# Optimization experiments

Measured on AMD Instinct MI355X. Metric: run time of the kernel, lower is better.

The kernel has to match this reference:

```python
import jax, jax.numpy as jnp
from jax import lax
import numpy as np

B = 262144   # batch of independent series
K = 64       # forecast horizon (init k)
D_IN = 200   # Non_AR_net input dim (Linear(200,100))
H = 100      # hidden width


def setup_inputs() -> dict:
    key = jax.random.key(0)
    ks = jax.random.split(key, 10)
    f32 = jnp.float32
    x = jax.random.normal(ks[0], (B, D_IN), f32)
    last_mu = jax.random.normal(ks[1], (B,), f32)
    # last_sigma is the variance state; keep it strictly positive
    last_sigma = jax.random.uniform(ks[2], (B,), f32) + 0.5
    # MLP params (Kaiming-ish scale)
    W1 = jax.random.normal(ks[3], (D_IN, H), f32) / np.float32(np.sqrt(D_IN))
    b1 = jnp.zeros((H,), f32)
    W2 = jax.random.normal(ks[4], (H, H), f32) / np.float32(np.sqrt(H))
    b2 = jnp.zeros((H,), f32)
    W3 = jax.random.normal(ks[5], (H, K), f32) / np.float32(np.sqrt(H))
    b3 = jnp.zeros((K,), f32)
    return {
        "x": x, "last_mu": last_mu, "last_sigma": last_sigma,
        "alpha_mu": jnp.asarray(0.1, f32), "alpha_sigma": jnp.asarray(0.1, f32),
        "beta_mu": jnp.asarray(0.9, f32), "beta_sigma": jnp.asarray(0.85, f32),
        "omega_mu": jnp.asarray(0.0, f32), "omega_sigma": jnp.asarray(0.05, f32),
        "nu": jnp.asarray(5.0, f32), "norm_strength": jnp.asarray(1.0, f32),
        "W1": W1, "b1": b1, "W2": W2, "b2": b2, "W3": W3, "b3": b3,
    }


def _mlp(x, W1, b1, W2, b2, W3, b3):
    h = jax.nn.relu(x @ W1 + b1)
    h = jax.nn.relu(h @ W2 + b2)
    return h @ W3 + b3  # [B, K]


def _ar_gas(deep_preds, last_mu, last_sigma, a_mu, a_s, b_mu, b_s, o_mu, o_s, nu, ns):
    """Student-t score-driven (GAS) k-step recurrence, vectorized over batch.
    deep_preds: [B, K]; state mu, sigma2: [B]."""
    w = 1.0 + 1.0 / nu

    def step(carry, y):  # y: [B]
        mu, s2 = carry
        e = y - mu
        denom = 1.0 + e * e / (nu * s2)
        mu_new = o_mu + ns * a_mu * (w * e / denom) + b_mu * mu
        s2_new = o_s + ns * a_s * (w * e * e / denom - s2) + b_s * s2
        return (mu_new, s2_new), (mu_new, s2_new)

    (_, _), (mus, s2s) = lax.scan(step, (last_mu, last_sigma), deep_preds.T)
    return mus.T, jnp.sqrt(s2s.T)  # [B, K] each


def reference(x, last_mu, last_sigma, alpha_mu, alpha_sigma, beta_mu, beta_sigma,
              omega_mu, omega_sigma, nu, norm_strength,
              W1, b1, W2, b2, W3, b3):
    deep_preds = _mlp(x, W1, b1, W2, b2, W3, b3)            # [B, K]
    dp = lax.stop_gradient(deep_preds)                       # .detach() in torch
    mu_pred, sigma_pred = _ar_gas(dp, last_mu, last_sigma,
                                  alpha_mu, alpha_sigma, beta_mu, beta_sigma,
                                  omega_mu, omega_sigma, nu, norm_strength)
    return deep_preds * sigma_pred + mu_pred                 # [B, K]
```

## Files before the change

### kernel.cpp

```cpp
#include <hip/hip_runtime.h>
#include <hip/hip_bf16.h>

typedef short v8s __attribute__((ext_vector_type(8)));
typedef float v4f __attribute__((ext_vector_type(4)));

#define THREADS 512
#define WAVES   8
#define NTILES  4
#define BMROWS  512
#define W1F     0
#define W2F     49
#define W3F     77
#define SLABB   95232
#define SLAB_STRIDE 264
#define SLAB_SIZE   4224
#define LDS_TOTAL   (SLABB + WAVES * SLAB_SIZE)

__device__ __forceinline__ unsigned short f2bf(float f) {
    union { __hip_bfloat16 h; unsigned short u; } c;
    c.h = __float2bfloat16(f);
    return c.u;
}
__device__ __forceinline__ unsigned pk2(float a, float b) {
    return (unsigned)f2bf(a) | ((unsigned)f2bf(b) << 16);
}
__device__ __forceinline__ v4f mfma16(v8s a, v8s b, v4f c) {
    return __builtin_amdgcn_mfma_f32_16x16x32_bf16(a, b, c, 0, 0, 0);
}
__device__ __forceinline__ v8s mkfrag(float4 a, float4 b) {
    union { unsigned u[4]; v8s s; } t;
    t.u[0] = pk2(a.x, a.y); t.u[1] = pk2(a.z, a.w);
    t.u[2] = pk2(b.x, b.y); t.u[3] = pk2(b.z, b.w);
    return t.s;
}
__device__ __forceinline__ void gload_lds16(const void* g, void* l) {
    __builtin_amdgcn_global_load_lds(
        (const __attribute__((address_space(1))) void*)g,
        (__attribute__((address_space(3))) void*)l, 16, 0, 0);
}

__global__ void prep_weights(const float* __restrict__ W1,
                             const float* __restrict__ W2,
                             const float* __restrict__ W3,
                             uint4* __restrict__ wf) {
    const int bid = blockIdx.x, l = threadIdx.x;
    const float* W; int K, N, KC, base, f;
    if (bid < 49)      { W = W1; K = 200; N = 100; KC = 7; base = W1F * 64; f = bid; }
    else if (bid < 77) { W = W2; K = 100; N = 100; KC = 4; base = W2F * 64; f = bid - 49; }
    else               { W = W3; K = 100; N = 64;  KC = 4; base = W3F * 64; f = bid - 77; }
    const int kc = f % KC;
    const int n  = (f / KC) * 16 + (l & 15);
    unsigned u[4];
    #pragma unroll
    for (int p = 0; p < 4; ++p) {
        const int k0 = kc * 32 + (l >> 4) * 8 + p * 2;
        const float a = (k0     < K && n < N) ? W[(size_t)k0 * N + n]       : 0.f;
        const float b = (k0 + 1 < K && n < N) ? W[(size_t)(k0 + 1) * N + n] : 0.f;
        u[p] = pk2(a, b);
    }
    wf[base + f * 64 + l] = make_uint4(u[0], u[1], u[2], u[3]);
}

__global__ __launch_bounds__(THREADS, 2)
void ar_gas_v18(const float* __restrict__ x,
                const float* __restrict__ last_mu,
                const float* __restrict__ last_sigma,
                const float* __restrict__ p_amu, const float* __restrict__ p_as,
                const float* __restrict__ p_bmu, const float* __restrict__ p_bs,
                const float* __restrict__ p_omu, const float* __restrict__ p_os,
                const float* __restrict__ p_nu,  const float* __restrict__ p_ns,
                const float* __restrict__ b1, const float* __restrict__ b2,
                const float* __restrict__ b3,
                const uint4* __restrict__ wf,
                float* __restrict__ out)
{
    extern __shared__ __align__(16) unsigned char L[];
    const int tid  = threadIdx.x;
    const int lane = tid & 63;
    const int wid  = tid >> 6;
    const int l15  = lane & 15;
    const int l4   = lane >> 4;
    const int blk  = blockIdx.x;

    const float anu = *p_nu,  ans = *p_ns;
    const float aMu = *p_amu, aSg = *p_as;
    const float bMu = *p_bmu, bSg = *p_bs;
    const float oMu = *p_omu, oSg = *p_os;
    const float wS  = 1.f + __builtin_amdgcn_rcpf(anu);
    const float cmu = ans * aMu * wS;
    const float cs  = ans * aSg * wS;
    const float bs2 = bSg - ans * aSg;

#define XLOADT(dst, base_row, kk)                                       \
    { int kb = (kk) * 32 + l4 * 8;                                      \
      kb = (kb + 8 <= 200) ? kb : 168;     \
      const float* p_ = x + ((base_row) + l15) * 200;                   \
      dst[kk][0] = *(const float4*)(p_ + kb);                           \
      dst[kk][1] = *(const float4*)(p_ + kb + 4); }

    const size_t gw0 = (size_t)blk * BMROWS + (size_t)wid * 64;

    float4 xv[7][2];
    #pragma unroll
    for (int kc = 0; kc < 7; ++kc) XLOADT(xv, gw0, kc);

    for (int s = wid; s < 93; s += WAVES)
        gload_lds16(wf + s * 64 + lane, L + s * 1024);
    __syncthreads();

#define FRAG_W1(f)  (*(const uint4*)(&L[(W1F + (f)) * 1024 + lane * 16]))
#define FRAG_W2(f)  (*(const uint4*)(&L[(W2F + (f)) * 1024 + lane * 16]))
#define FRAG_W3(f)  (*(const uint4*)(&L[(W3F + (f)) * 1024 + lane * 16]))

    const int sb      = SLABB + wid * SLAB_SIZE;
    const int sb_epi  = sb + (l4 * 4) * SLAB_STRIDE + l15 * 2;
    const int sb_rd   = sb + l15 * SLAB_STRIDE + l4 * 16;
    const int sb_dpw  = sb + (l4 * 4) * SLAB_STRIDE + l15 * 4;
    const int sb_gas  = sb + l15 * SLAB_STRIDE;
    const int sb_st   = sb + l4 * SLAB_STRIDE + l15 * 16;

    #pragma unroll 1
    for (int t = 0; t < NTILES; ++t) {
        const size_t gw = gw0 + t * 16;

        const float mu_init = last_mu[gw + l15];
        const float s2_init = last_sigma[gw + l15];

        v4f acc[7];
        #pragma unroll
        for (int nt = 0; nt < 7; ++nt) acc[nt] = (v4f){0.f, 0.f, 0.f, 0.f};
        #pragma unroll
        for (int kc = 0; kc < 7; ++kc) {
            uint4 bu[7];
            #pragma unroll
            for (int nt = 0; nt < 7; ++nt) bu[nt] = FRAG_W1(nt * 7 + kc);
            const v8s af = mkfrag(xv[kc][0], xv[kc][1]);
            #pragma unroll
            for (int nt = 0; nt < 7; ++nt)
                acc[nt] = mfma16(af, *(const v8s*)&bu[nt], acc[nt]);
        }

        if (t < NTILES - 1) {
            #pragma unroll
            for (int kc = 0; kc < 7; ++kc) XLOADT(xv, gw0 + (t + 1) * 16, kc);
        }

        {
            float bv[7];
            #pragma unroll
            for (int nt = 0; nt < 7; ++nt) {
                const int c = nt * 16 + l15;
                bv[nt] = (c < 100) ? b1[c] : 0.f;
            }
            #pragma unroll
            for (int nt = 0; nt < 7; ++nt)
                #pragma unroll
                for (int r = 0; r < 4; ++r) {
                    const float v = fmaxf(acc[nt][r] + bv[nt], 0.f);
                    *(unsigned short*)(&L[sb_epi + r * SLAB_STRIDE + nt * 32]) =
                        f2bf(v);
                }
        }
        if (lane < 32)
            *(uint4*)(&L[sb + (lane >> 1) * SLAB_STRIDE + 224 + (lane & 1) * 16]) =
                make_uint4(0, 0, 0, 0);

        v4f acc2[7];
        #pragma unroll
        for (int nt = 0; nt < 7; ++nt) acc2[nt] = (v4f){0.f, 0.f, 0.f, 0.f};
        #pragma unroll
        for (int kc = 0; kc < 4; ++kc) {
            uint4 bu[7];
            #pragma unroll
            for (int nt = 0; nt < 7; ++nt) bu[nt] = FRAG_W2(nt * 4 + kc);
            uint4 t0 = *(const uint4*)(&L[sb_rd + kc * 64]);
            const v8s af = *(v8s*)&t0;
            #pragma unroll
            for (int nt = 0; nt < 7; ++nt)
                acc2[nt] = mfma16(af, *(const v8s*)&bu[nt], acc2[nt]);
        }
        {
            float bv[7];
            #pragma unroll
            for (int nt = 0; nt < 7; ++nt) {
                const int c = nt * 16 + l15;
                bv[nt] = (c < 100) ? b2[c] : 0.f;
            }
            #pragma unroll
            for (int nt = 0; nt < 7; ++nt)
                #pragma unroll
                for (int r = 0; r < 4; ++r) {
                    const float v = fmaxf(acc2[nt][r] + bv[nt], 0.f);
                    *(unsigned short*)(&L[sb_epi + r * SLAB_STRIDE + nt * 32]) =
                        f2bf(v);
                }
        }

        v4f acc3[4];
        #pragma unroll
        for (int nt = 0; nt < 4; ++nt) acc3[nt] = (v4f){0.f, 0.f, 0.f, 0.f};
        #pragma unroll
        for (int kc = 0; kc < 4; ++kc) {
            uint4 bu[4];
            #pragma unroll
            for (int nt = 0; nt < 4; ++nt) bu[nt] = FRAG_W3(nt * 4 + kc);
            uint4 t0 = *(const uint4*)(&L[sb_rd + kc * 64]);
            const v8s af = *(v8s*)&t0;
            #pragma unroll
            for (int nt = 0; nt < 4; ++nt)
                acc3[nt] = mfma16(af, *(const v8s*)&bu[nt], acc3[nt]);
        }
        {
            float bv[4];
            #pragma unroll
            for (int nt = 0; nt < 4; ++nt) bv[nt] = b3[nt * 16 + l15];
            #pragma unroll
            for (int nt = 0; nt < 4; ++nt)
                #pragma unroll
                for (int r = 0; r < 4; ++r)
                    *(float*)(&L[sb_dpw + r * SLAB_STRIDE + nt * 64]) =
                        acc3[nt][r] + bv[nt];
        }

        if (lane < 16) {
            float mu = mu_init;
            float s2 = s2_init;
#define GAS_STEP(Y, O)                                                  \
            {   const float e    = (Y) - mu;                            \
                const float nus2 = anu * s2;                            \
                const float den  = fmaf(e, e, nus2);                    \
                const float r0   = __builtin_amdgcn_rcpf(den);          \
                const float p    = e * nus2 * r0;                       \
                mu = fmaf(cmu, p, fmaf(bMu, mu, oMu));                  \
                s2 = fmaf(cs, e * p, fmaf(bs2, s2, oSg));               \
                (O) = fmaf((Y), __builtin_amdgcn_sqrtf(s2), mu); }
            #pragma unroll
            for (int q = 0; q < 16; ++q) {
                float4 d = *(float4*)(&L[sb_gas + q * 16]);
                float o0, o1, o2, o3;
                GAS_STEP(d.x, o0); GAS_STEP(d.y, o1);
                GAS_STEP(d.z, o2); GAS_STEP(d.w, o3);
                *(float4*)(&L[sb_gas + q * 16]) = make_float4(o0, o1, o2, o3);
            }
#undef GAS_STEP
        }

        #pragma unroll
        for (int i = 0; i < 4; ++i) {
            float4 v = *(float4*)(&L[sb_st + i * (4 * SLAB_STRIDE)]);
            ((float4*)out)[gw * 16 + i * 64 + lane] = v;
        }
    }
#undef FRAG_W1
#undef FRAG_W2
#undef FRAG_W3
#undef XLOADT
}

extern "C" void kernel_launch(void* const* d_in, const int* in_sizes, int n_in,
                              void* d_out, int out_size, void* d_ws, size_t ws_size,
                              hipStream_t stream) {
    const float* x          = (const float*)d_in[0];
    const float* last_mu    = (const float*)d_in[1];
    const float* last_sigma = (const float*)d_in[2];
    const float* amu        = (const float*)d_in[3];
    const float* asig       = (const float*)d_in[4];
    const float* bmu        = (const float*)d_in[5];
    const float* bsig       = (const float*)d_in[6];
    const float* omu        = (const float*)d_in[7];
    const float* osig       = (const float*)d_in[8];
    const float* nu         = (const float*)d_in[9];
    const float* ns         = (const float*)d_in[10];
    const float* W1         = (const float*)d_in[11];
    const float* b1         = (const float*)d_in[12];
    const float* W2         = (const float*)d_in[13];
    const float* b2         = (const float*)d_in[14];
    const float* W3         = (const float*)d_in[15];
    const float* b3         = (const float*)d_in[16];
    float* out = (float*)d_out;

    uint4* wf = (uint4*)d_ws;
    prep_weights<<<93, 64, 0, stream>>>(W1, W2, W3, wf);

    hipFuncSetAttribute((const void*)ar_gas_v18,
                        hipFuncAttributeMaxDynamicSharedMemorySize, LDS_TOTAL);

    const int B = in_sizes[1];
    dim3 grid(B / BMROWS), block(THREADS);
    ar_gas_v18<<<grid, block, LDS_TOTAL, stream>>>(
        x, last_mu, last_sigma,
        amu, asig, bmu, bsig, omu, osig, nu, ns,
        b1, b2, b3, wf, out);
}
```

Before: 83.29 us.

## Split fused MLP+GAS kernel into MLP kernel and per-row scan kernel

```diff
diff --git a/kernel.cpp b/kernel.cpp
--- a/kernel.cpp
+++ b/kernel.cpp
@@ -4,17 +4,17 @@
 typedef short v8s __attribute__((ext_vector_type(8)));
 typedef float v4f __attribute__((ext_vector_type(4)));
 
-#define THREADS 512
-#define WAVES   8
-#define NTILES  4
-#define BMROWS  512
+#define A_THREADS 1024
+#define A_WAVES   16
+#define A_NTILES  4
+#define A_ROWS    1024
 #define W1F     0
 #define W2F     49
 #define W3F     77
 #define SLABB   95232
-#define SLAB_STRIDE 264
-#define SLAB_SIZE   4224
-#define LDS_TOTAL   (SLABB + WAVES * SLAB_SIZE)
+#define SLAB_STRIDE 260
+#define SLAB_SIZE   4160
+#define LDS_TOTAL   (SLABB + A_WAVES * SLAB_SIZE)
 
 __device__ __forceinline__ unsigned short f2bf(float f) {
     union { __hip_bfloat16 h; unsigned short u; } c;
@@ -61,18 +61,12 @@
     wf[base + f * 64 + l] = make_uint4(u[0], u[1], u[2], u[3]);
 }
 
-__global__ __launch_bounds__(THREADS, 2)
-void ar_gas_v18(const float* __restrict__ x,
-                const float* __restrict__ last_mu,
-                const float* __restrict__ last_sigma,
-                const float* __restrict__ p_amu, const float* __restrict__ p_as,
-                const float* __restrict__ p_bmu, const float* __restrict__ p_bs,
-                const float* __restrict__ p_omu, const float* __restrict__ p_os,
-                const float* __restrict__ p_nu,  const float* __restrict__ p_ns,
-                const float* __restrict__ b1, const float* __restrict__ b2,
-                const float* __restrict__ b3,
-                const uint4* __restrict__ wf,
-                float* __restrict__ out)
+__global__ __launch_bounds__(A_THREADS, 4)
+void ar_mlp(const float* __restrict__ x,
+            const float* __restrict__ b1, const float* __restrict__ b2,
+            const float* __restrict__ b3,
+            const uint4* __restrict__ wf,
+            float* __restrict__ dp)
 {
     extern __shared__ __align__(16) unsigned char L[];
     const int tid  = threadIdx.x;
@@ -82,29 +76,21 @@
     const int l4   = lane >> 4;
     const int blk  = blockIdx.x;
 
-    const float anu = *p_nu,  ans = *p_ns;
-    const float aMu = *p_amu, aSg = *p_as;
-    const float bMu = *p_bmu, bSg = *p_bs;
-    const float oMu = *p_omu, oSg = *p_os;
-    const float wS  = 1.f + __builtin_amdgcn_rcpf(anu);
-    const float cmu = ans * aMu * wS;
-    const float cs  = ans * aSg * wS;
-    const float bs2 = bSg - ans * aSg;
-
-#define XLOADT(dst, base_row, kk)                                       \
+#define XLOAD(d0, d1, base_row, kk)                                     \
     { int kb = (kk) * 32 + l4 * 8;                                      \
       kb = (kb + 8 <= 200) ? kb : 168;     \
       const float* p_ = x + ((base_row) + l15) * 200;                   \
-      dst[kk][0] = *(const float4*)(p_ + kb);                           \
-      dst[kk][1] = *(const float4*)(p_ + kb + 4); }
-
-    const size_t gw0 = (size_t)blk * BMROWS + (size_t)wid * 64;
-
-    float4 xv[7][2];
-    #pragma unroll
-    for (int kc = 0; kc < 7; ++kc) XLOADT(xv, gw0, kc);
-
-    for (int s = wid; s < 93; s += WAVES)
+      d0 = *(const float4*)(p_ + kb);                                   \
+      d1 = *(const float4*)(p_ + kb + 4); }
+
+    const size_t gw0 = (size_t)blk * A_ROWS + (size_t)wid * 64;
+
+    float4 xv[3][2];
+    XLOAD(xv[0][0], xv[0][1], gw0, 0);
+    XLOAD(xv[1][0], xv[1][1], gw0, 1);
+    XLOAD(xv[2][0], xv[2][1], gw0, 2);
+
+    for (int s = wid; s < 93; s += A_WAVES)
         gload_lds16(wf + s * 64 + lane, L + s * 1024);
     __syncthreads();
 
@@ -115,16 +101,10 @@
     const int sb      = SLABB + wid * SLAB_SIZE;
     const int sb_epi  = sb + (l4 * 4) * SLAB_STRIDE + l15 * 2;
     const int sb_rd   = sb + l15 * SLAB_STRIDE + l4 * 16;
-    const int sb_dpw  = sb + (l4 * 4) * SLAB_STRIDE + l15 * 4;
-    const int sb_gas  = sb + l15 * SLAB_STRIDE;
-    const int sb_st   = sb + l4 * SLAB_STRIDE + l15 * 16;
 
     #pragma unroll 1
-    for (int t = 0; t < NTILES; ++t) {
+    for (int t = 0; t < A_NTILES; ++t) {
         const size_t gw = gw0 + t * 16;
-
-        const float mu_init = last_mu[gw + l15];
-        const float s2_init = last_sigma[gw + l15];
 
         v4f acc[7];
         #pragma unroll
@@ -134,15 +114,16 @@
             uint4 bu[7];
             #pragma unroll
             for (int nt = 0; nt < 7; ++nt) bu[nt] = FRAG_W1(nt * 7 + kc);
-            const v8s af = mkfrag(xv[kc][0], xv[kc][1]);
+            const v8s af = mkfrag(xv[kc % 3][0], xv[kc % 3][1]);
+            if (kc < 4) XLOAD(xv[kc % 3][0], xv[kc % 3][1], gw, kc + 3);
             #pragma unroll
             for (int nt = 0; nt < 7; ++nt)
                 acc[nt] = mfma16(af, *(const v8s*)&bu[nt], acc[nt]);
         }
-
-        if (t < NTILES - 1) {
-            #pragma unroll
-            for (int kc = 0; kc < 7; ++kc) XLOADT(xv, gw0 + (t + 1) * 16, kc);
+        if (t < A_NTILES - 1) {
+            XLOAD(xv[0][0], xv[0][1], gw + 16, 0);
+            XLOAD(xv[1][0], xv[1][1], gw + 16, 1);
+            XLOAD(xv[2][0], xv[2][1], gw + 16, 2);
         }
 
         {
@@ -218,43 +199,66 @@
             for (int nt = 0; nt < 4; ++nt)
                 #pragma unroll
                 for (int r = 0; r < 4; ++r)
-                    *(float*)(&L[sb_dpw + r * SLAB_STRIDE + nt * 64]) =
+                    dp[(gw + l4 * 4 + r) * 64 + nt * 16 + l15] =
                         acc3[nt][r] + bv[nt];
-        }
-
-        if (lane < 16) {
-            float mu = mu_init;
-            float s2 = s2_init;
-#define GAS_STEP(Y, O)                                                  \
-            {   const float e    = (Y) - mu;                            \
-                const float nus2 = anu * s2;                            \
-                const float den  = fmaf(e, e, nus2);                    \
-                const float r0   = __builtin_amdgcn_rcpf(den);          \
-                const float p    = e * nus2 * r0;                       \
-                mu = fmaf(cmu, p, fmaf(bMu, mu, oMu));                  \
-                s2 = fmaf(cs, e * p, fmaf(bs2, s2, oSg));               \
-                (O) = fmaf((Y), __builtin_amdgcn_sqrtf(s2), mu); }
-            #pragma unroll
-            for (int q = 0; q < 16; ++q) {
-                float4 d = *(float4*)(&L[sb_gas + q * 16]);
-                float o0, o1, o2, o3;
-                GAS_STEP(d.x, o0); GAS_STEP(d.y, o1);
-                GAS_STEP(d.z, o2); GAS_STEP(d.w, o3);
-                *(float4*)(&L[sb_gas + q * 16]) = make_float4(o0, o1, o2, o3);
-            }
-#undef GAS_STEP
-        }
-
-        #pragma unroll
-        for (int i = 0; i < 4; ++i) {
-            float4 v = *(float4*)(&L[sb_st + i * (4 * SLAB_STRIDE)]);
-            ((float4*)out)[gw * 16 + i * 64 + lane] = v;
         }
     }
 #undef FRAG_W1
 #undef FRAG_W2
 #undef FRAG_W3
-#undef XLOADT
+#undef XLOAD
+}
+
+__global__ void ar_gas_scan(float* __restrict__ io,
+                            const float* __restrict__ last_mu,
+                            const float* __restrict__ last_sigma,
+                            const float* __restrict__ p_amu,
+                            const float* __restrict__ p_as,
+                            const float* __restrict__ p_bmu,
+                            const float* __restrict__ p_bs,
+                            const float* __restrict__ p_omu,
+                            const float* __restrict__ p_os,
+                            const float* __restrict__ p_nu,
+                            const float* __restrict__ p_ns)
+{
+    const int row = blockIdx.x * 256 + threadIdx.x;
+    float4* rp = (float4*)(io + (size_t)row * 64);
+
+    const float anu = *p_nu,  ans = *p_ns;
+    const float aMu = *p_amu, aSg = *p_as;
+    const float bMu = *p_bmu, bSg = *p_bs;
+    const float oMu = *p_omu, oSg = *p_os;
+    const float w   = 1.f + __builtin_amdgcn_rcpf(anu);
+    const float cmu = ans * aMu * w;
+    const float cs  = ans * aSg * w;
+    const float bs2 = bSg - ans * aSg;
+
+    float mu = last_mu[row];
+    float s2 = last_sigma[row];
+
+    float4 c[16];
+    c[0] = rp[0]; c[1] = rp[1];
+
+#define GAS_STEP(Y, O)                                                  \
+    {   const float e    = (Y) - mu;                                    \
+        const float nus2 = anu * s2;                                    \
+        const float den  = fmaf(e, e, nus2);                            \
+        const float r0   = __builtin_amdgcn_rcpf(den);                  \
+        const float p    = e * nus2 * r0;                               \
+        mu = fmaf(cmu, p, fmaf(bMu, mu, oMu));                          \
+        s2 = fmaf(cs, e * p, fmaf(bs2, s2, oSg));                       \
+        (O) = fmaf((Y), __builtin_amdgcn_sqrtf(s2), mu); }
+
+    #pragma unroll
+    for (int q = 0; q < 16; ++q) {
+        if (q + 2 < 16) c[q + 2] = rp[q + 2];
+        float4 d = c[q];
+        float o0, o1, o2, o3;
+        GAS_STEP(d.x, o0); GAS_STEP(d.y, o1);
+        GAS_STEP(d.z, o2); GAS_STEP(d.w, o3);
+        rp[q] = make_float4(o0, o1, o2, o3);
+    }
+#undef GAS_STEP
 }
 
 extern "C" void kernel_launch(void* const* d_in, const int* in_sizes, int n_in,
@@ -282,13 +286,13 @@
     uint4* wf = (uint4*)d_ws;
     prep_weights<<<93, 64, 0, stream>>>(W1, W2, W3, wf);
 
-    hipFuncSetAttribute((const void*)ar_gas_v18,
+    hipFuncSetAttribute((const void*)ar_mlp,
                         hipFuncAttributeMaxDynamicSharedMemorySize, LDS_TOTAL);
 
     const int B = in_sizes[1];
-    dim3 grid(B / BMROWS), block(THREADS);
-    ar_gas_v18<<<grid, block, LDS_TOTAL, stream>>>(
-        x, last_mu, last_sigma,
-        amu, asig, bmu, bsig, omu, osig, nu, ns,
-        b1, b2, b3, wf, out);
-}
+    ar_mlp<<<dim3(B / A_ROWS), dim3(A_THREADS), LDS_TOTAL, stream>>>(
+        x, b1, b2, b3, wf, out);
+    ar_gas_scan<<<dim3(B / 256), dim3(256), 0, stream>>>(
+        out, last_mu, last_sigma,
+        amu, asig, bmu, bsig, omu, osig, nu, ns);
+}
```

Measured after the change: 131.9 us. 58.3% more time.

## Software-pipeline GAS recurrence of previous tile into next tile's layer-1 MFMA loop

Applied to the files above, without the earlier changes.

```diff
diff --git a/kernel.cpp b/kernel.cpp
--- a/kernel.cpp
+++ b/kernel.cpp
@@ -62,7 +62,7 @@
 }
 
 __global__ __launch_bounds__(THREADS, 2)
-void ar_gas_v18(const float* __restrict__ x,
+void ar_gas_v21(const float* __restrict__ x,
                 const float* __restrict__ last_mu,
                 const float* __restrict__ last_sigma,
                 const float* __restrict__ p_amu, const float* __restrict__ p_as,
@@ -119,12 +119,32 @@
     const int sb_gas  = sb + l15 * SLAB_STRIDE;
     const int sb_st   = sb + l4 * SLAB_STRIDE + l15 * 16;
 
+    float  mu_g = 0.f, s2_g = 1.f;
+    size_t gw_prev = 0;
+
+#define GAS_STEP(Y, O)                                                  \
+    {   const float e    = (Y) - mu_g;                                  \
+        const float nus2 = anu * s2_g;                                  \
+        const float den  = fmaf(e, e, nus2);                            \
+        const float r0   = __builtin_amdgcn_rcpf(den);                  \
+        const float p    = e * nus2 * r0;                               \
+        mu_g = fmaf(cmu, p, fmaf(bMu, mu_g, oMu));                      \
+        s2_g = fmaf(cs, e * p, fmaf(bs2, s2_g, oSg));                   \
+        (O) = fmaf((Y), __builtin_amdgcn_sqrtf(s2_g), mu_g); }
+
+#define GAS_Q(q)                                                        \
+    if (doGas) {                                                        \
+        float4 d = *(float4*)(&L[sb_gas + (q) * 16]);                   \
+        float o0, o1, o2, o3;                                           \
+        GAS_STEP(d.x, o0); GAS_STEP(d.y, o1);                           \
+        GAS_STEP(d.z, o2); GAS_STEP(d.w, o3);                           \
+        *(float4*)(&L[sb_gas + (q) * 16]) = make_float4(o0, o1, o2, o3);\
+    }
+
     #pragma unroll 1
     for (int t = 0; t < NTILES; ++t) {
         const size_t gw = gw0 + t * 16;
-
-        const float mu_init = last_mu[gw + l15];
-        const float s2_init = last_sigma[gw + l15];
+        const bool doGas = (t > 0) && (lane < 16);
 
         v4f acc[7];
         #pragma unroll
@@ -135,15 +155,30 @@
             #pragma unroll
             for (int nt = 0; nt < 7; ++nt) bu[nt] = FRAG_W1(nt * 7 + kc);
             const v8s af = mkfrag(xv[kc][0], xv[kc][1]);
+            GAS_Q(2 * kc);
+            GAS_Q(2 * kc + 1);
             #pragma unroll
             for (int nt = 0; nt < 7; ++nt)
                 acc[nt] = mfma16(af, *(const v8s*)&bu[nt], acc[nt]);
         }
+        GAS_Q(14);
+        GAS_Q(15);
+        if (t > 0) {
+            #pragma unroll
+            for (int i = 0; i < 4; ++i) {
+                float4 v = *(float4*)(&L[sb_st + i * (4 * SLAB_STRIDE)]);
+                ((float4*)out)[gw_prev * 16 + i * 64 + lane] = v;
+            }
+        }
 
         if (t < NTILES - 1) {
             #pragma unroll
-            for (int kc = 0; kc < 7; ++kc) XLOADT(xv, gw0 + (t + 1) * 16, kc);
-        }
+            for (int kc = 0; kc < 7; ++kc) XLOADT(xv, gw + 16, kc);
+        }
+
+        mu_g = last_mu[gw + l15];
+        s2_g = last_sigma[gw + l15];
+        gw_prev = gw;
 
         {
             float bv[7];
@@ -221,36 +256,20 @@
                     *(float*)(&L[sb_dpw + r * SLAB_STRIDE + nt * 64]) =
                         acc3[nt][r] + bv[nt];
         }
-
-        if (lane < 16) {
-            float mu = mu_init;
-            float s2 = s2_init;
-#define GAS_STEP(Y, O)                                                  \
-            {   const float e    = (Y) - mu;                            \
-                const float nus2 = anu * s2;                            \
-                const float den  = fmaf(e, e, nus2);                    \
-                const float r0   = __builtin_amdgcn_rcpf(den);          \
-                const float p    = e * nus2 * r0;                       \
-                mu = fmaf(cmu, p, fmaf(bMu, mu, oMu));                  \
-                s2 = fmaf(cs, e * p, fmaf(bs2, s2, oSg));               \
-                (O) = fmaf((Y), __builtin_amdgcn_sqrtf(s2), mu); }
-            #pragma unroll
-            for (int q = 0; q < 16; ++q) {
-                float4 d = *(float4*)(&L[sb_gas + q * 16]);
-                float o0, o1, o2, o3;
-                GAS_STEP(d.x, o0); GAS_STEP(d.y, o1);
-                GAS_STEP(d.z, o2); GAS_STEP(d.w, o3);
-                *(float4*)(&L[sb_gas + q * 16]) = make_float4(o0, o1, o2, o3);
-            }
-#undef GAS_STEP
-        }
-
+    }
+
+    {
+        const bool doGas = (lane < 16);
+        #pragma unroll
+        for (int q = 0; q < 16; ++q) { GAS_Q(q); }
         #pragma unroll
         for (int i = 0; i < 4; ++i) {
             float4 v = *(float4*)(&L[sb_st + i * (4 * SLAB_STRIDE)]);
-            ((float4*)out)[gw * 16 + i * 64 + lane] = v;
+            ((float4*)out)[gw_prev * 16 + i * 64 + lane] = v;
         }
     }
+#undef GAS_Q
+#undef GAS_STEP
 #undef FRAG_W1
 #undef FRAG_W2
 #undef FRAG_W3
@@ -282,12 +301,12 @@
     uint4* wf = (uint4*)d_ws;
     prep_weights<<<93, 64, 0, stream>>>(W1, W2, W3, wf);
 
-    hipFuncSetAttribute((const void*)ar_gas_v18,
+    hipFuncSetAttribute((const void*)ar_gas_v21,
                         hipFuncAttributeMaxDynamicSharedMemorySize, LDS_TOTAL);
 
     const int B = in_sizes[1];
     dim3 grid(B / BMROWS), block(THREADS);
-    ar_gas_v18<<<grid, block, LDS_TOTAL, stream>>>(
+    ar_gas_v21<<<grid, block, LDS_TOTAL, stream>>>(
         x, last_mu, last_sigma,
         amu, asig, bmu, bsig, omu, osig, nu, ns,
         b1, b2, b3, wf, out);
```

New measurement: 88.22 us. +5.9%, slower.
